# Optimization experiments

Measured on AMD Instinct MI355X. Metric: run time of the kernel, lower is better.

The kernel has to match this reference:

```python
import jax, jax.numpy as jnp
import numpy as np

QMAX = 127.0  # torch.iinfo(torch.int8).max


def setup_inputs() -> dict:
    key = jax.random.key(0)
    k1, k2 = jax.random.split(key)
    input_act = jax.random.normal(k1, (4, 2048, 4096), dtype=jnp.float32)
    # nn.Linear weight: [out_features, in_features], fp weights pre-quantization
    weight = jax.random.normal(k2, (4096, 4096), dtype=jnp.float32) * 0.02
    return {"input_act": input_act, "weight": weight}


def reference(input_act, weight):
    # --- weight_quant (per-channel over in_features) ---
    w_scale = jnp.max(jnp.abs(weight), axis=-1, keepdims=True) / QMAX      # [O, 1]
    w_q = jnp.round(weight / w_scale).astype(jnp.int8)                      # int8 weight

    # --- activation quant (per-token over last dim) ---
    a_scale = jnp.max(jnp.abs(input_act), axis=-1, keepdims=True) / QMAX    # [B, S, 1]
    x_q = jnp.round(input_act / a_scale).astype(jnp.int8)                   # int8 acts

    # --- int8 GEMM with int32 accumulation (torch._int_mm semantics) ---
    # [B, S, K] @ [K, O] -> [B, S, O]
    acc = jnp.matmul(x_q.astype(jnp.int32), w_q.T.astype(jnp.int32))        # exact int32

    # --- dequant: scale = input_act_scale * weight_scale.T, then cast to fp16 ---
    scale = a_scale * w_scale.T[None, :, :]                                 # [B, S, O]
    out = (acc.astype(jnp.float32) * scale).astype(jnp.float16)
    return out
```

## Files before the change

### kernel.cpp

```cpp
#include <hip/hip_runtime.h>
#include <hip/hip_fp16.h>
#include <cstdint>

typedef int v4i __attribute__((ext_vector_type(4)));

#define AS1C(p) ((const __attribute__((address_space(1))) void*)(p))
#define AS3(p)  ((__attribute__((address_space(3))) void*)(p))

__global__ __launch_bounds__(256) void quant_fused(const float* __restrict__ X,
                                                   const float* __restrict__ W,
                                                   int8_t* __restrict__ Xq,
                                                   int8_t* __restrict__ Wq,
                                                   float* __restrict__ a_scale,
                                                   float* __restrict__ w_scale) {
    const int row = blockIdx.x;
    const float* src;
    int8_t* dst;
    float* scp;
    if (row < 8192) {
        src = X + (size_t)row * 4096;  dst = Xq + (size_t)row * 4096;  scp = a_scale + row;
    } else {
        const int r = row - 8192;
        src = W + (size_t)r * 4096;    dst = Wq + (size_t)r * 4096;    scp = w_scale + r;
    }
    const float4* xv = (const float4*)src;

    float4 v[4];
#pragma unroll
    for (int j = 0; j < 4; ++j) v[j] = xv[threadIdx.x + (j << 8)];

    float m = 0.0f;
#pragma unroll
    for (int j = 0; j < 4; ++j) {
        m = fmaxf(m, fmaxf(fmaxf(fabsf(v[j].x), fabsf(v[j].y)),
                           fmaxf(fabsf(v[j].z), fabsf(v[j].w))));
    }
    for (int off = 32; off > 0; off >>= 1)
        m = fmaxf(m, __shfl_xor(m, off, 64));

    __shared__ float wmax[4];
    __shared__ float s_sc;
    const int lane = threadIdx.x & 63;
    const int wv = threadIdx.x >> 6;
    if (lane == 0) wmax[wv] = m;
    __syncthreads();
    if (threadIdx.x == 0) {
        float mm = fmaxf(fmaxf(wmax[0], wmax[1]), fmaxf(wmax[2], wmax[3]));
        float sc = mm / 127.0f;
        *scp = sc;
        s_sc = sc;
    }
    __syncthreads();
    const float sc = s_sc;

    char4* qv = (char4*)dst;
#pragma unroll
    for (int j = 0; j < 4; ++j) {
        char4 q;
        q.x = (signed char)(int)rintf(v[j].x / sc);
        q.y = (signed char)(int)rintf(v[j].y / sc);
        q.z = (signed char)(int)rintf(v[j].z / sc);
        q.w = (signed char)(int)rintf(v[j].w / sc);
        qv[threadIdx.x + (j << 8)] = q;
    }
}

__global__ __launch_bounds__(512, 2) void gemm_i8(const int8_t* __restrict__ Aq,
                                                  const int8_t* __restrict__ Bq,
                                                  const float* __restrict__ a_scale,
                                                  const float* __restrict__ w_scale,
                                                  float* __restrict__ out) {
    extern __shared__ __align__(16) int8_t smem[];

    const int K = 4096;
    const int bid = blockIdx.x;
    const int wg  = (bid & 7) * 64 + (bid >> 3);
    const int n0 = (wg & 15) * 256;
    const int m0 = (wg >> 4) * 256;

    const int tid  = threadIdx.x;
    const int lane = tid & 63;
    const int wid  = tid >> 6;
    const int wm   = wid >> 2;
    const int wn   = wid & 3;

    const int rsel  = lane & 15;
    const int kswz  = ((lane >> 4) << 4) ^ (((rsel >> 1) & 3) << 4);
    const int abase = (wm * 128 + rsel) * 64 + kswz;
    const int bbase = 16384 + (wn * 64 + rsel) * 64 + kswz;

    const int strow = tid >> 2;
    const int stswz = ((strow >> 1) & 3) << 4;
    const int stcol = ((tid & 3) << 4) ^ stswz;
    const int8_t* gA = Aq + (size_t)(m0 + strow) * K + stcol;
    const int8_t* gB = Bq + (size_t)(n0 + strow) * K + stcol;
    const size_t rstep = (size_t)128 * K;
    const int ldsst = wid * 1024;

    v4i acc[8][4] = {};
    v4i aFa[8], aFb[8], bFa[4], bFb[4];

#define STAGE(buf, kt) do {                                                          \
    int8_t* _d = smem + (buf) * 32768;                                               \
    const int8_t* _a = gA + (size_t)(kt) * 64;                                       \
    const int8_t* _b = gB + (size_t)(kt) * 64;                                       \
    __builtin_amdgcn_global_load_lds(AS1C(_a),         AS3(_d + ldsst),         16, 0, 0); \
    __builtin_amdgcn_global_load_lds(AS1C(_a + rstep), AS3(_d + 8192  + ldsst), 16, 0, 0); \
    __builtin_amdgcn_global_load_lds(AS1C(_b),         AS3(_d + 16384 + ldsst), 16, 0, 0); \
    __builtin_amdgcn_global_load_lds(AS1C(_b + rstep), AS3(_d + 24576 + ldsst), 16, 0, 0); \
  } while (0)

#define READS(g, NA, NB, gsrc, goff) do {                                            \
    NA[2*(g)]     = *(const v4i*)(bufN + abase + (2*(g))     * 1024);                \
    NA[2*(g) + 1] = *(const v4i*)(bufN + abase + (2*(g) + 1) * 1024);                \
    NB[(g)]       = *(const v4i*)(bufN + bbase + (g) * 1024);                        \
    __builtin_amdgcn_global_load_lds(AS1C(gsrc), AS3(pD + (goff) + ldsst), 16, 0, 0);\
  } while (0)

#define MFMAS(g, CA, CB) do {                                                        \
    __builtin_amdgcn_s_setprio(1);                                                   \
    _Pragma("unroll")                                                                \
    for (int nt = 0; nt < 4; ++nt) {                                                 \
        acc[2*(g)][nt] = __builtin_amdgcn_mfma_i32_16x16x64_i8(                      \
            CA[2*(g)], CB[nt], acc[2*(g)][nt], 0, 0, 0);                             \
        acc[2*(g)+1][nt] = __builtin_amdgcn_mfma_i32_16x16x64_i8(                    \
            CA[2*(g)+1], CB[nt], acc[2*(g)+1][nt], 0, 0, 0);                         \
    }                                                                                \
    __builtin_amdgcn_s_setprio(0);                                                   \
  } while (0)

#define GROUP_RW(g, CA, CB, NA, NB, gsrc, goff)  do {                                \
    READS(g, NA, NB, gsrc, goff);                                                    \
    __builtin_amdgcn_sched_barrier(0);                                               \
    MFMAS(g, CA, CB);                                                                \
    __builtin_amdgcn_sched_barrier(0);                                               \
  } while (0)

#define GROUP_WR(g, CA, CB, NA, NB, gsrc, goff)  do {                                \
    MFMAS(g, CA, CB);                                                                \
    __builtin_amdgcn_sched_barrier(0);                                               \
    READS(g, NA, NB, gsrc, goff);                                                    \
    __builtin_amdgcn_sched_barrier(0);                                               \
  } while (0)

#define KSTEP(G, u, CA, CB, NA, NB, kt4) do {                                        \
    const int kt  = (kt4) + (u);                                                     \
    const int8_t* bufN = smem + (((u) + 1) & 3) * 32768;                             \
    int8_t* pD = smem + (((u) + 3) & 3) * 32768;                                     \
    const int ktp = (kt + 3 < 64) ? (kt + 3) : 63;                                   \
    const int8_t* _a = gA + (size_t)ktp * 64;                                        \
    const int8_t* _b = gB + (size_t)ktp * 64;                                        \
    asm volatile("s_waitcnt vmcnt(4)" ::: "memory");                                 \
    __builtin_amdgcn_s_barrier();                                                    \
    __builtin_amdgcn_sched_barrier(0);                                               \
    G(0, CA, CB, NA, NB, _a,         0);                                             \
    G(1, CA, CB, NA, NB, _a + rstep, 8192);                                          \
    G(2, CA, CB, NA, NB, _b,         16384);                                         \
    G(3, CA, CB, NA, NB, _b + rstep, 24576);                                         \
  } while (0)

    STAGE(0, 0); STAGE(1, 1); STAGE(2, 2);
    asm volatile("s_waitcnt vmcnt(8)" ::: "memory");
    __builtin_amdgcn_s_barrier();
#pragma unroll
    for (int mt = 0; mt < 8; ++mt) aFa[mt] = *(const v4i*)(smem + abase + mt * 1024);
#pragma unroll
    for (int nt = 0; nt < 4; ++nt) bFa[nt] = *(const v4i*)(smem + bbase + nt * 1024);

    if (wid < 4) {
        for (int kt4 = 0; kt4 < 64; kt4 += 4) {
            KSTEP(GROUP_RW, 0, aFa, bFa, aFb, bFb, kt4);
            KSTEP(GROUP_RW, 1, aFb, bFb, aFa, bFa, kt4);
            KSTEP(GROUP_RW, 2, aFa, bFa, aFb, bFb, kt4);
            KSTEP(GROUP_RW, 3, aFb, bFb, aFa, bFa, kt4);
        }
    } else {
        for (int kt4 = 0; kt4 < 64; kt4 += 4) {
            KSTEP(GROUP_WR, 0, aFa, bFa, aFb, bFb, kt4);
            KSTEP(GROUP_WR, 1, aFb, bFb, aFa, bFa, kt4);
            KSTEP(GROUP_WR, 2, aFa, bFa, aFb, bFb, kt4);
            KSTEP(GROUP_WR, 3, aFb, bFb, aFa, bFa, kt4);
        }
    }

    const int r0  = (lane >> 4) << 2;
    const int col = lane & 15;
#pragma unroll
    for (int mt = 0; mt < 8; ++mt) {
        const int tbase = m0 + wm * 128 + mt * 16 + r0;
        float as[4];
#pragma unroll
        for (int r = 0; r < 4; ++r) as[r] = a_scale[tbase + r];
#pragma unroll
        for (int nt = 0; nt < 4; ++nt) {
            const int o = n0 + wn * 64 + nt * 16 + col;
            const float wsc = w_scale[o];
#pragma unroll
            for (int r = 0; r < 4; ++r) {
                float v = (float)acc[mt][nt][r] * as[r] * wsc;
                out[(size_t)(tbase + r) * 4096 + o] = __half2float(__float2half_rn(v));
            }
        }
    }
#undef KSTEP
#undef GROUP_RW
#undef GROUP_WR
#undef MFMAS
#undef READS
#undef STAGE
}

extern "C" void kernel_launch(void* const* d_in, const int* in_sizes, int n_in,
                              void* d_out, int out_size, void* d_ws, size_t ws_size,
                              hipStream_t stream) {
    const float* input_act = (const float*)d_in[0];
    const float* weight    = (const float*)d_in[1];
    float* out = (float*)d_out;

    const int K = 4096, O = 4096, T = 8192;

    int8_t* x_q = (int8_t*)d_ws;
    int8_t* w_q = x_q + (size_t)T * K;
    float* a_scale = (float*)(w_q + (size_t)O * K);
    float* w_scale = a_scale + T;

    static bool attr_done = false;
    if (!attr_done) {
        hipFuncSetAttribute(reinterpret_cast<const void*>(gemm_i8),
                            hipFuncAttributeMaxDynamicSharedMemorySize, 131072);
        attr_done = true;
    }

    quant_fused<<<T + O, 256, 0, stream>>>(input_act, weight, x_q, w_q,
                                           a_scale, w_scale);

    dim3 grid(512);
    gemm_i8<<<grid, 512, 131072, stream>>>(x_q, w_q, a_scale, w_scale, out);
}
```

Baseline: 177.1 us.

## Replace ping-pong register double-buffering with per-phase barrier-synchronized LDS read+MFMA

Drops the register double-buffered fragments (aFa/aFb, bFa/bFb) and the split-warp ping-pong (RW vs WR ordering by warp id). Each k-step now runs four phases; each phase reads fragments from the current LDS buffer, issues one global->LDS prefetch, barriers, waits for LDS, runs its MFMAs, then barriers again. This cuts register pressure and makes all warps follow one schedule, but it adds two barriers per phase and serializes LDS reads ahead of MFMAs, losing the read/compute overlap.

```diff
diff --git a/kernel.cpp b/kernel.cpp
--- a/kernel.cpp
+++ b/kernel.cpp
@@ -98,89 +98,66 @@
     const int ldsst = wid * 1024;
 
     v4i acc[8][4] = {};
-    v4i aFa[8], aFb[8], bFa[4], bFb[4];
+    v4i aF[8], bF[4];
 
 #define STAGE(buf, kt) do {                                                          \
     int8_t* _d = smem + (buf) * 32768;                                               \
-    const int8_t* _a = gA + (size_t)(kt) * 64;                                       \
-    const int8_t* _b = gB + (size_t)(kt) * 64;                                       \
-    __builtin_amdgcn_global_load_lds(AS1C(_a),         AS3(_d + ldsst),         16, 0, 0); \
-    __builtin_amdgcn_global_load_lds(AS1C(_a + rstep), AS3(_d + 8192  + ldsst), 16, 0, 0); \
-    __builtin_amdgcn_global_load_lds(AS1C(_b),         AS3(_d + 16384 + ldsst), 16, 0, 0); \
-    __builtin_amdgcn_global_load_lds(AS1C(_b + rstep), AS3(_d + 24576 + ldsst), 16, 0, 0); \
+    const int8_t* _sa = gA + (size_t)(kt) * 64;                                      \
+    const int8_t* _sb = gB + (size_t)(kt) * 64;                                      \
+    __builtin_amdgcn_global_load_lds(AS1C(_sa),         AS3(_d + ldsst),         16, 0, 0); \
+    __builtin_amdgcn_global_load_lds(AS1C(_sa + rstep), AS3(_d + 8192  + ldsst), 16, 0, 0); \
+    __builtin_amdgcn_global_load_lds(AS1C(_sb),         AS3(_d + 16384 + ldsst), 16, 0, 0); \
+    __builtin_amdgcn_global_load_lds(AS1C(_sb + rstep), AS3(_d + 24576 + ldsst), 16, 0, 0); \
   } while (0)
 
-#define READS(g, NA, NB, gsrc, goff) do {                                            \
-    NA[2*(g)]     = *(const v4i*)(bufN + abase + (2*(g))     * 1024);                \
-    NA[2*(g) + 1] = *(const v4i*)(bufN + abase + (2*(g) + 1) * 1024);                \
-    NB[(g)]       = *(const v4i*)(bufN + bbase + (g) * 1024);                        \
+#define PHASE(q, gsrc, goff, last) do {                                              \
+    if ((q) == 0) {                                                                  \
+        bF[0] = *(const v4i*)(bufc + bbase);                                         \
+        bF[1] = *(const v4i*)(bufc + bbase + 1024);                                  \
+        bF[2] = *(const v4i*)(bufc + bbase + 2048);                                  \
+        bF[3] = *(const v4i*)(bufc + bbase + 3072);                                  \
+    }                                                                                \
+    aF[2*(q)]     = *(const v4i*)(bufc + abase + (2*(q))     * 1024);                \
+    aF[2*(q) + 1] = *(const v4i*)(bufc + abase + (2*(q) + 1) * 1024);                \
     __builtin_amdgcn_global_load_lds(AS1C(gsrc), AS3(pD + (goff) + ldsst), 16, 0, 0);\
-  } while (0)
-
-#define MFMAS(g, CA, CB) do {                                                        \
+    __builtin_amdgcn_s_barrier();                                                    \
+    asm volatile("s_waitcnt lgkmcnt(0)" ::: "memory");                               \
+    __builtin_amdgcn_sched_barrier(0);                                               \
     __builtin_amdgcn_s_setprio(1);                                                   \
     _Pragma("unroll")                                                                \
     for (int nt = 0; nt < 4; ++nt) {                                                 \
-        acc[2*(g)][nt] = __builtin_amdgcn_mfma_i32_16x16x64_i8(                      \
-            CA[2*(g)], CB[nt], acc[2*(g)][nt], 0, 0, 0);                             \
-        acc[2*(g)+1][nt] = __builtin_amdgcn_mfma_i32_16x16x64_i8(                    \
-            CA[2*(g)+1], CB[nt], acc[2*(g)+1][nt], 0, 0, 0);                         \
+        acc[2*(q)][nt] = __builtin_amdgcn_mfma_i32_16x16x64_i8(                      \
+            aF[2*(q)], bF[nt], acc[2*(q)][nt], 0, 0, 0);                             \
+        acc[2*(q)+1][nt] = __builtin_amdgcn_mfma_i32_16x16x64_i8(                    \
+            aF[2*(q)+1], bF[nt], acc[2*(q)+1][nt], 0, 0, 0);                         \
     }                                                                                \
     __builtin_amdgcn_s_setprio(0);                                                   \
+    if (last) asm volatile("s_waitcnt vmcnt(8)" ::: "memory");                       \
+    __builtin_amdgcn_s_barrier();                                                    \
   } while (0)
 
-#define GROUP_RW(g, CA, CB, NA, NB, gsrc, goff)  do {                                \
-    READS(g, NA, NB, gsrc, goff);                                                    \
-    __builtin_amdgcn_sched_barrier(0);                                               \
-    MFMAS(g, CA, CB);                                                                \
-    __builtin_amdgcn_sched_barrier(0);                                               \
-  } while (0)
-
-#define GROUP_WR(g, CA, CB, NA, NB, gsrc, goff)  do {                                \
-    MFMAS(g, CA, CB);                                                                \
-    __builtin_amdgcn_sched_barrier(0);                                               \
-    READS(g, NA, NB, gsrc, goff);                                                    \
-    __builtin_amdgcn_sched_barrier(0);                                               \
-  } while (0)
-
-#define KSTEP(G, u, CA, CB, NA, NB, kt4) do {                                        \
+#define KSTEP(u, kt4) do {                                                           \
     const int kt  = (kt4) + (u);                                                     \
-    const int8_t* bufN = smem + (((u) + 1) & 3) * 32768;                             \
+    const int8_t* bufc = smem + (u) * 32768;                                         \
     int8_t* pD = smem + (((u) + 3) & 3) * 32768;                                     \
     const int ktp = (kt + 3 < 64) ? (kt + 3) : 63;                                   \
     const int8_t* _a = gA + (size_t)ktp * 64;                                        \
     const int8_t* _b = gB + (size_t)ktp * 64;                                        \
-    asm volatile("s_waitcnt vmcnt(4)" ::: "memory");                                 \
-    __builtin_amdgcn_s_barrier();                                                    \
-    __builtin_amdgcn_sched_barrier(0);                                               \
-    G(0, CA, CB, NA, NB, _a,         0);                                             \
-    G(1, CA, CB, NA, NB, _a + rstep, 8192);                                          \
-    G(2, CA, CB, NA, NB, _b,         16384);                                         \
-    G(3, CA, CB, NA, NB, _b + rstep, 24576);                                         \
+    PHASE(0, _a,         0,     0);                                                  \
+    PHASE(1, _a + rstep, 8192,  0);                                                  \
+    PHASE(2, _b,         16384, 0);                                                  \
+    PHASE(3, _b + rstep, 24576, 1);                                                  \
   } while (0)
 
     STAGE(0, 0); STAGE(1, 1); STAGE(2, 2);
     asm volatile("s_waitcnt vmcnt(8)" ::: "memory");
     __builtin_amdgcn_s_barrier();
-#pragma unroll
-    for (int mt = 0; mt < 8; ++mt) aFa[mt] = *(const v4i*)(smem + abase + mt * 1024);
-#pragma unroll
-    for (int nt = 0; nt < 4; ++nt) bFa[nt] = *(const v4i*)(smem + bbase + nt * 1024);
-
-    if (wid < 4) {
-        for (int kt4 = 0; kt4 < 64; kt4 += 4) {
-            KSTEP(GROUP_RW, 0, aFa, bFa, aFb, bFb, kt4);
-            KSTEP(GROUP_RW, 1, aFb, bFb, aFa, bFa, kt4);
-            KSTEP(GROUP_RW, 2, aFa, bFa, aFb, bFb, kt4);
-            KSTEP(GROUP_RW, 3, aFb, bFb, aFa, bFa, kt4);
-        }
-    } else {
-        for (int kt4 = 0; kt4 < 64; kt4 += 4) {
-            KSTEP(GROUP_WR, 0, aFa, bFa, aFb, bFb, kt4);
-            KSTEP(GROUP_WR, 1, aFb, bFb, aFa, bFa, kt4);
-            KSTEP(GROUP_WR, 2, aFa, bFa, aFb, bFb, kt4);
-            KSTEP(GROUP_WR, 3, aFb, bFb, aFa, bFa, kt4);
-        }
+
+    for (int kt4 = 0; kt4 < 64; kt4 += 4) {
+        KSTEP(0, kt4);
+        KSTEP(1, kt4);
+        KSTEP(2, kt4);
+        KSTEP(3, kt4);
     }
 
     const int r0  = (lane >> 4) << 2;
@@ -203,10 +180,7 @@
         }
     }
 #undef KSTEP
-#undef GROUP_RW
-#undef GROUP_WR
-#undef MFMAS
-#undef READS
+#undef PHASE
 #undef STAGE
 }
 
```

Result: slower. 186.3 us (+5.2%).
